# Optimization experiments

Hardware: AMD Instinct MI355X
Metric: run time of the kernel (lower is better)

Reference implementation:

```python
import jax, jax.numpy as jnp
import numpy as np

B, N, NINP, NFEAT, H = 4096, 4096, 64, 32, 4


def setup_inputs() -> dict:
    key = jax.random.key(0)
    ks = jax.random.split(key, 8)
    s_in = 1.0 / np.sqrt(NINP)
    s_att = 1.0 / np.sqrt(2 * NFEAT)
    return {
        "X": jax.random.normal(ks[0], (B, NINP), jnp.float32),
        "G": jax.random.normal(ks[1], (N, NINP), jnp.float32),
        "A": jax.random.uniform(ks[2], (B, N), jnp.float32),  # additive mask
        "W": jax.random.uniform(ks[3], (H, NINP, NFEAT), jnp.float32, -s_in, s_in),
        "b": jax.random.uniform(ks[4], (H, NFEAT), jnp.float32, -s_in, s_in),
        "a_src": jax.random.uniform(ks[5], (H, NFEAT), jnp.float32, -s_att, s_att),
        "a_dst": jax.random.uniform(ks[6], (H, NFEAT), jnp.float32, -s_att, s_att),
        "att_b": jax.random.uniform(ks[7], (H,), jnp.float32, -s_att, s_att),
    }


def reference(X, G, A, W, b, a_src, a_dst, att_b):
    # Per-head linear transforms (all heads batched via einsum)
    WX = jnp.einsum("bi,hif->bhf", X, W) + b            # (B, H, F)
    WG = jnp.einsum("ni,hif->nhf", G, W) + b            # (N, H, F)
    # Decomposed concat-attention: a^T [WX_b ; WG_n] = a_src.WX_b + a_dst.WG_n
    s_src = jnp.einsum("bhf,hf->bh", WX, a_src)         # (B, H)
    s_dst = jnp.einsum("nhf,hf->nh", WG, a_dst)         # (N, H)
    e = s_src[:, :, None] + s_dst.T[None, :, :] + att_b[None, :, None]  # (B,H,N)
    att = jax.nn.softmax(e - A[:, None, :], axis=-1)    # adjacency-masked softmax
    # Dropout(0.5) is identity in eval mode (deterministic reference).
    out = jnp.einsum("bhn,nhf->bhf", att, WG)           # weighted aggregation
    out = jax.nn.relu(out)                              # activation before concat
    return out.reshape(out.shape[0], -1)                # (B, H*F) concat heads
```

## Files before the change

### kernel.cpp

```cpp
#include <hip/hip_runtime.h>
#include <stdint.h>

#define N_TOK 4096
#define D_IN  64
#define NF    32
#define NH    4
#define OUTW  (NH * NF)
#define NT    8
#define CHUNK 128
#define BT    32

typedef float        f32x4  __attribute__((ext_vector_type(4)));
typedef unsigned int uint4v __attribute__((ext_vector_type(4)));
typedef __bf16       bf16x8 __attribute__((ext_vector_type(8)));

union Frag { uint4v u; bf16x8 v; };

static __device__ __forceinline__ unsigned short f2bf_rne(float x) {
  unsigned u = __float_as_uint(x);
  u += 0x7fffu + ((u >> 16) & 1u);
  return (unsigned short)(u >> 16);
}
static __device__ __forceinline__ float bflo(unsigned x) {
  return __uint_as_float(x << 16);
}
static __device__ __forceinline__ float bfhi(unsigned x) {
  return __uint_as_float(x & 0xffff0000u);
}

__global__ __launch_bounds__(128) void prep_kernel(
    const float* __restrict__ G, const float* __restrict__ W,
    const float* __restrict__ bias, const float* __restrict__ a_dst,
    unsigned short* __restrict__ EDH, unsigned short* __restrict__ PB) {
  __shared__ float gs[NT * D_IN];
  const int tid = threadIdx.x;
  const int n0  = blockIdx.x * NT;
  {
    const float4* src = (const float4*)(G + (size_t)n0 * D_IN);
    float4* dst = (float4*)gs;
    dst[tid] = src[tid];
  }
  __syncthreads();
  const int h = tid >> 5, f = tid & 31;
  float acc[NT];
  const float bb = bias[h * NF + f];
#pragma unroll
  for (int k = 0; k < NT; ++k) acc[k] = bb;
#pragma unroll
  for (int i = 0; i < D_IN; ++i) {
    const float wv = W[(h * D_IN + i) * NF + f];
#pragma unroll
    for (int k = 0; k < NT; ++k) acc[k] = fmaf(gs[k * D_IN + i], wv, acc[k]);
  }
  const float ad = a_dst[h * NF + f];
  float ev[NT];
#pragma unroll
  for (int k = 0; k < NT; ++k) {
    float s = acc[k] * ad;
    s += __shfl_xor(s, 1);  s += __shfl_xor(s, 2);  s += __shfl_xor(s, 4);
    s += __shfl_xor(s, 8);  s += __shfl_xor(s, 16);
    ev[k] = __expf(s);
  }
  const int t   = n0 >> 5;
  const int gq  = (n0 >> 3) & 3;
  const int set = (h << 1) | (f >> 4);
  const int col = f & 15;
  union { uint4 u4; unsigned short us[8]; } pk;
#pragma unroll
  for (int k = 0; k < NT; ++k) pk.us[k] = f2bf_rne(acc[k] * ev[k]);
  *(uint4*)(PB + (size_t)((((t * 8 + set) << 6) + (gq << 4) + col)) * 8) = pk.u4;
  if (f == 0) {
    union { uint4 u4; unsigned short us[8]; } pe;
#pragma unroll
    for (int k = 0; k < NT; ++k) pe.us[k] = f2bf_rne(ev[k]);
    *(uint4*)&EDH[(size_t)h * N_TOK + n0] = pe.u4;
  }
}

template <int NS>
__global__ __launch_bounds__(512) void attn_kernel(
    const float* __restrict__ A, const unsigned short* __restrict__ EDH,
    const unsigned short* __restrict__ PB, float* __restrict__ op,
    float* __restrict__ dp, float* __restrict__ out) {
  constexpr int NHALF  = N_TOK / NS;
  constexpr int NIT    = NHALF / CHUNK;
  constexpr int RINGSZ = BT * CHUNK * 2;
  __shared__ __align__(16) unsigned short ring[3 * BT * CHUNK];
  __shared__ __align__(16) unsigned short EDt[NH * NHALF];
  __shared__ float denLds[BT * NH];
  char* ringb = (char*)ring;

  const int tid  = threadIdx.x;
  const int lane = tid & 63;
  const int w    = tid >> 6;
  const int bid  = blockIdx.x;
  const int s    = bid & (NS - 1);
  const int b0   = (bid / NS) * BT;

  const int srow = tid >> 4, tp = tid & 15;
  const float* abase = A + (size_t)(b0 + srow) * N_TOK + s * NHALF + tp * 8;
  const int wb0 = srow * 256 + ((tp ^ (srow & 15)) << 4);

  const int rowm = lane & 15, g = lane >> 4;
  const char* pbb  = (const char*)PB + (size_t)s * (NHALF / 32) * 8192;
  const char* pown = pbb + (((w << 6) + lane) << 4);

  {
    const uint4* src = (const uint4*)EDH;
    uint4* dst = (uint4*)EDt;
    constexpr int tot = NH * NHALF / 8;
#pragma unroll 1
    for (int i = tid; i < tot; i += 512) {
      const int hh = i / (NHALF / 8), k = i % (NHALF / 8);
      dst[i] = src[hh * (N_TOK / 8) + s * (NHALF / 8) + k];
    }
  }
  __syncthreads();

  f32x4 acc0 = {0.f, 0.f, 0.f, 0.f}, acc1 = {0.f, 0.f, 0.f, 0.f};
  f32x4 dsum = {0.f, 0.f, 0.f, 0.f};
  f32x4 aXa, aXb, aYa, aYb;
  Frag bo0, bo1, bo2, bo3, co0, co1, co2, co3;
  int mR = 0, mW = 1;

#define LOADA2(d0, d1, cc) do {                                                \
    const float* ap_ = abase + (size_t)(cc) * CHUNK;                           \
    asm volatile("global_load_dwordx4 %0, %1, off"                            \
                 : "=v"(d0) : "v"(ap_) : "memory");                            \
    asm volatile("global_load_dwordx4 %0, %1, off"                            \
                 : "=v"(d1) : "v"(ap_ + 4) : "memory");                        \
  } while (0)
#define LOADB(fr, cc, kk)                                                      \
  asm volatile("global_load_dwordx4 %0, %1, off"                              \
               : "=v"(fr.u)                                                    \
               : "v"(pown + (size_t)((cc) * 4 + (kk)) * 8192) : "memory")

#define EXPP(AV0, AV1, cchunk, mw) do {                                        \
    float x0 = __expf(-AV0[0]), x1 = __expf(-AV0[1]);                          \
    float x2 = __expf(-AV0[2]), x3 = __expf(-AV0[3]);                          \
    float x4 = __expf(-AV1[0]), x5 = __expf(-AV1[1]);                          \
    float x6 = __expf(-AV1[2]), x7 = __expf(-AV1[3]);                          \
    if ((cchunk) < NIT) {                                                      \
      const int eo_ = (cchunk) * CHUNK + tp * 8;                               \
      uint4v e0_ = *(const uint4v*)&EDt[0 * NHALF + eo_];                      \
      uint4v e1_ = *(const uint4v*)&EDt[1 * NHALF + eo_];                      \
      uint4v e2_ = *(const uint4v*)&EDt[2 * NHALF + eo_];                      \
      uint4v e3_ = *(const uint4v*)&EDt[3 * NHALF + eo_];                      \
      dsum[0] = fmaf(x0, bflo(e0_[0]), dsum[0]);                               \
      dsum[0] = fmaf(x1, bfhi(e0_[0]), dsum[0]);                               \
      dsum[0] = fmaf(x2, bflo(e0_[1]), dsum[0]);                               \
      dsum[0] = fmaf(x3, bfhi(e0_[1]), dsum[0]);                               \
      dsum[0] = fmaf(x4, bflo(e0_[2]), dsum[0]);                               \
      dsum[0] = fmaf(x5, bfhi(e0_[2]), dsum[0]);                               \
      dsum[0] = fmaf(x6, bflo(e0_[3]), dsum[0]);                               \
      dsum[0] = fmaf(x7, bfhi(e0_[3]), dsum[0]);                               \
      dsum[1] = fmaf(x0, bflo(e1_[0]), dsum[1]);                               \
      dsum[1] = fmaf(x1, bfhi(e1_[0]), dsum[1]);                               \
      dsum[1] = fmaf(x2, bflo(e1_[1]), dsum[1]);                               \
      dsum[1] = fmaf(x3, bfhi(e1_[1]), dsum[1]);                               \
      dsum[1] = fmaf(x4, bflo(e1_[2]), dsum[1]);                               \
      dsum[1] = fmaf(x5, bfhi(e1_[2]), dsum[1]);                               \
      dsum[1] = fmaf(x6, bflo(e1_[3]), dsum[1]);                               \
      dsum[1] = fmaf(x7, bfhi(e1_[3]), dsum[1]);                               \
      dsum[2] = fmaf(x0, bflo(e2_[0]), dsum[2]);                               \
      dsum[2] = fmaf(x1, bfhi(e2_[0]), dsum[2]);                               \
      dsum[2] = fmaf(x2, bflo(e2_[1]), dsum[2]);                               \
      dsum[2] = fmaf(x3, bfhi(e2_[1]), dsum[2]);                               \
      dsum[2] = fmaf(x4, bflo(e2_[2]), dsum[2]);                               \
      dsum[2] = fmaf(x5, bfhi(e2_[2]), dsum[2]);                               \
      dsum[2] = fmaf(x6, bflo(e2_[3]), dsum[2]);                               \
      dsum[2] = fmaf(x7, bfhi(e2_[3]), dsum[2]);                               \
      dsum[3] = fmaf(x0, bflo(e3_[0]), dsum[3]);                               \
      dsum[3] = fmaf(x1, bfhi(e3_[0]), dsum[3]);                               \
      dsum[3] = fmaf(x2, bflo(e3_[1]), dsum[3]);                               \
      dsum[3] = fmaf(x3, bfhi(e3_[1]), dsum[3]);                               \
      dsum[3] = fmaf(x4, bflo(e3_[2]), dsum[3]);                               \
      dsum[3] = fmaf(x5, bfhi(e3_[2]), dsum[3]);                               \
      dsum[3] = fmaf(x6, bflo(e3_[3]), dsum[3]);                               \
      dsum[3] = fmaf(x7, bfhi(e3_[3]), dsum[3]);                               \
    }                                                                          \
    uint4v t_;                                                                 \
    t_[0] = __builtin_amdgcn_perm(__float_as_uint(x1), __float_as_uint(x0), 0x07060302u); \
    t_[1] = __builtin_amdgcn_perm(__float_as_uint(x3), __float_as_uint(x2), 0x07060302u); \
    t_[2] = __builtin_amdgcn_perm(__float_as_uint(x5), __float_as_uint(x4), 0x07060302u); \
    t_[3] = __builtin_amdgcn_perm(__float_as_uint(x7), __float_as_uint(x6), 0x07060302u); \
    *(uint4v*)(ringb + (mw) * RINGSZ + wb0) = t_;                              \
  } while (0)

#define MSTEP(rg, kk, FB) do {                                                 \
    Frag af_;                                                                  \
    af_.v = *(const bf16x8*)(ringb + mR * RINGSZ + ((rg) * 16 + rowm) * 256 +  \
                             ((((kk) * 4 + g) ^ rowm) << 4));                  \
    if ((rg) == 0)                                                             \
      acc0 = __builtin_amdgcn_mfma_f32_16x16x32_bf16(af_.v, FB.v, acc0, 0, 0, 0); \
    else                                                                       \
      acc1 = __builtin_amdgcn_mfma_f32_16x16x32_bf16(af_.v, FB.v, acc1, 0, 0, 0); \
  } while (0)

#define ITER(cc, AC0, AC1, AN0, AN1, CO0, CO1, CO2, CO3,                       \
             NO0, NO1, NO2, NO3) do {                                          \
    { const int cb_ = ((cc) + 1 < NIT) ? (cc) + 1 : NIT - 1;                   \
      LOADB(NO0, cb_, 0); LOADB(NO1, cb_, 1);                                  \
      LOADB(NO2, cb_, 2); LOADB(NO3, cb_, 3); }                                \
    { const int ca_ = ((cc) + 2 < NIT) ? (cc) + 2 : NIT - 1;                   \
      LOADA2(AN0, AN1, ca_); }                                                 \
    asm volatile("s_waitcnt vmcnt(6)" ::: "memory");                           \
    __builtin_amdgcn_sched_barrier(0);                                         \
    EXPP(AC0, AC1, (cc) + 1, mW);                                              \
    asm volatile("s_waitcnt lgkmcnt(0)" ::: "memory");                         \
    __builtin_amdgcn_sched_barrier(0);                                         \
    __builtin_amdgcn_s_barrier();                                              \
    MSTEP(0, 0, CO0); MSTEP(1, 0, CO0);                                        \
    MSTEP(0, 1, CO1); MSTEP(1, 1, CO1);                                        \
    MSTEP(0, 2, CO2); MSTEP(1, 2, CO2);                                        \
    MSTEP(0, 3, CO3); MSTEP(1, 3, CO3);                                        \
    mR = mW; mW = (mW + 1 == 3) ? 0 : mW + 1;                                  \
  } while (0)

  LOADA2(aXa, aXb, 0);
  LOADB(bo0, 0, 0); LOADB(bo1, 0, 1); LOADB(bo2, 0, 2); LOADB(bo3, 0, 3);
  LOADA2(aYa, aYb, 1);
  asm volatile("s_waitcnt vmcnt(6)" ::: "memory");
  __builtin_amdgcn_sched_barrier(0);
  EXPP(aXa, aXb, 0, 0);

#pragma unroll 1
  for (int i = 0; i < NIT; i += 2) {
    ITER(i,     aYa, aYb, aXa, aXb, bo0, bo1, bo2, bo3, co0, co1, co2, co3);
    ITER(i + 1, aXa, aXb, aYa, aYb, co0, co1, co2, co3, bo0, bo1, bo2, bo3);
  }

  asm volatile("s_waitcnt vmcnt(0)" ::: "memory");
  __builtin_amdgcn_sched_barrier(0);

#pragma unroll
  for (int m = 1; m <= 8; m <<= 1) {
    dsum[0] += __shfl_xor(dsum[0], m);
    dsum[1] += __shfl_xor(dsum[1], m);
    dsum[2] += __shfl_xor(dsum[2], m);
    dsum[3] += __shfl_xor(dsum[3], m);
  }

  if (NS == 1) {
    if (tp == 0) {
      float4 dv; dv.x = dsum[0]; dv.y = dsum[1]; dv.z = dsum[2]; dv.w = dsum[3];
      *(float4*)&denLds[srow * NH] = dv;
    }
    __syncthreads();
    const int hh = w >> 1;
#pragma unroll
    for (int r = 0; r < 4; ++r) {
      const int rr = g * 4 + r;
      float o;
      o = acc0[r] / denLds[rr * NH + hh];
      out[(size_t)(b0 + rr) * OUTW + w * 16 + rowm] = o > 0.f ? o : 0.f;
      o = acc1[r] / denLds[(16 + rr) * NH + hh];
      out[(size_t)(b0 + 16 + rr) * OUTW + w * 16 + rowm] = o > 0.f ? o : 0.f;
    }
  } else {
    if (tp == 0) {
      float4 dv; dv.x = dsum[0]; dv.y = dsum[1]; dv.z = dsum[2]; dv.w = dsum[3];
      *(float4*)&dp[((size_t)s * N_TOK + b0 + srow) * NH] = dv;
    }
    float* ob = op + (size_t)s * (N_TOK * OUTW) + (size_t)b0 * OUTW + w * 16 + rowm;
#pragma unroll
    for (int r = 0; r < 4; ++r) {
      const int rr = g * 4 + r;
      ob[(size_t)rr * OUTW]        = acc0[r];
      ob[(size_t)(16 + rr) * OUTW] = acc1[r];
    }
  }
#undef LOADA2
#undef LOADB
#undef EXPP
#undef MSTEP
#undef ITER
}

__global__ __launch_bounds__(256) void comb_kernel(
    const float* __restrict__ op, const float* __restrict__ dp,
    float* __restrict__ out, int NS) {
  const int idx4 = blockIdx.x * 256 + threadIdx.x;
  const int eb = idx4 >> 5;
  const int h  = ((idx4 << 2) & 127) >> 5;
  float4 o; o.x = 0.f; o.y = 0.f; o.z = 0.f; o.w = 0.f;
  float d = 0.f;
  for (int s2 = 0; s2 < NS; ++s2) {
    float4 vv = *(const float4*)(op + (size_t)s2 * (N_TOK * OUTW) + (size_t)idx4 * 4);
    o.x += vv.x; o.y += vv.y; o.z += vv.z; o.w += vv.w;
    d += dp[((size_t)s2 * N_TOK + eb) * NH + h];
  }
  const float r = 1.f / d;
  float4 res;
  res.x = fmaxf(o.x * r, 0.f);
  res.y = fmaxf(o.y * r, 0.f);
  res.z = fmaxf(o.z * r, 0.f);
  res.w = fmaxf(o.w * r, 0.f);
  *(float4*)(out + (size_t)idx4 * 4) = res;
}

extern "C" void kernel_launch(void* const* d_in, const int* in_sizes, int n_in,
                              void* d_out, int out_size, void* d_ws, size_t ws_size,
                              hipStream_t stream) {
  const float* G     = (const float*)d_in[1];
  const float* A     = (const float*)d_in[2];
  const float* W     = (const float*)d_in[3];
  const float* bias  = (const float*)d_in[4];
  const float* a_dst = (const float*)d_in[6];

  char* ws = (char*)d_ws;
  const size_t PBsz = (size_t)128 * 8 * 1024;
  const size_t EDsz = (size_t)N_TOK * NH * 2;
  const size_t base = PBsz + EDsz;
  const size_t per_split = (size_t)N_TOK * OUTW * 4 + (size_t)N_TOK * NH * 4;

  unsigned short* PB  = (unsigned short*)ws;
  unsigned short* EDH = (unsigned short*)(ws + PBsz);
  float* op = (float*)(ws + base);
  float* outp = (float*)d_out;

  prep_kernel<<<N_TOK / NT, 128, 0, stream>>>(G, W, bias, a_dst, EDH, PB);
  if (ws_size >= base + 8 * per_split) {
    float* dp = (float*)(ws + base + 8 * (size_t)N_TOK * OUTW * 4);
    attn_kernel<8><<<(N_TOK / BT) * 8, 512, 0, stream>>>(A, EDH, PB, op, dp, nullptr);
    comb_kernel<<<(N_TOK * OUTW / 4) / 256, 256, 0, stream>>>(op, dp, outp, 8);
  } else if (ws_size >= base + 4 * per_split) {
    float* dp = (float*)(ws + base + 4 * (size_t)N_TOK * OUTW * 4);
    attn_kernel<4><<<(N_TOK / BT) * 4, 512, 0, stream>>>(A, EDH, PB, op, dp, nullptr);
    comb_kernel<<<(N_TOK * OUTW / 4) / 256, 256, 0, stream>>>(op, dp, outp, 4);
  } else if (ws_size >= base + 2 * per_split) {
    float* dp = (float*)(ws + base + 2 * (size_t)N_TOK * OUTW * 4);
    attn_kernel<2><<<(N_TOK / BT) * 2, 512, 0, stream>>>(A, EDH, PB, op, dp, nullptr);
    comb_kernel<<<(N_TOK * OUTW / 4) / 256, 256, 0, stream>>>(op, dp, outp, 2);
  } else {
    attn_kernel<1><<<N_TOK / BT, 512, 0, stream>>>(A, EDH, PB, nullptr, nullptr, outp);
  }
}
```

Before: 34.14 us.

## Halve attention block to 256 threads, each wave computing two output column tiles

The attention kernel now runs 4 waves per block instead of 8. Each wave owns two 16-column output tiles and reuses every LDS A-fragment for two MFMAs, so LDS reads per MFMA are halved. Each thread also exponentiates 16 mask values instead of 8. The B-fragment prefetch changes from double-buffered next-chunk loading to loading the current chunk inside the iteration, guarded by a vmcnt wait before the MFMAs. In exchange the kernel uses more registers per thread, has fewer waves to hide latency, and may expose the B-load latency.

```diff
diff --git a/kernel.cpp b/kernel.cpp
--- a/kernel.cpp
+++ b/kernel.cpp
@@ -78,7 +78,7 @@
 }
 
 template <int NS>
-__global__ __launch_bounds__(512) void attn_kernel(
+__global__ __launch_bounds__(256) void attn_kernel(
     const float* __restrict__ A, const unsigned short* __restrict__ EDH,
     const unsigned short* __restrict__ PB, float* __restrict__ op,
     float* __restrict__ dp, float* __restrict__ out) {
@@ -97,55 +97,65 @@
   const int s    = bid & (NS - 1);
   const int b0   = (bid / NS) * BT;
 
-  const int srow = tid >> 4, tp = tid & 15;
-  const float* abase = A + (size_t)(b0 + srow) * N_TOK + s * NHALF + tp * 8;
-  const int wb0 = srow * 256 + ((tp ^ (srow & 15)) << 4);
+  const int srow = tid >> 3, tp = tid & 7;
+  const float* abase = A + (size_t)(b0 + srow) * N_TOK + s * NHALF + tp * 16;
+  const int wb0 = srow * 256 + (((2 * tp    ) ^ (srow & 15)) << 4);
+  const int wb1 = srow * 256 + (((2 * tp + 1) ^ (srow & 15)) << 4);
 
   const int rowm = lane & 15, g = lane >> 4;
-  const char* pbb  = (const char*)PB + (size_t)s * (NHALF / 32) * 8192;
-  const char* pown = pbb + (((w << 6) + lane) << 4);
+  const char* pbb = (const char*)PB + (size_t)s * (NHALF / 32) * 8192;
+  const char* pw0 = pbb + ((((2 * w    ) << 6) + lane) << 4);
+  const char* pw1 = pbb + ((((2 * w + 1) << 6) + lane) << 4);
 
   {
     const uint4* src = (const uint4*)EDH;
     uint4* dst = (uint4*)EDt;
     constexpr int tot = NH * NHALF / 8;
 #pragma unroll 1
-    for (int i = tid; i < tot; i += 512) {
+    for (int i = tid; i < tot; i += 256) {
       const int hh = i / (NHALF / 8), k = i % (NHALF / 8);
       dst[i] = src[hh * (N_TOK / 8) + s * (NHALF / 8) + k];
     }
   }
   __syncthreads();
 
-  f32x4 acc0 = {0.f, 0.f, 0.f, 0.f}, acc1 = {0.f, 0.f, 0.f, 0.f};
+  f32x4 ac00 = {0.f, 0.f, 0.f, 0.f}, ac01 = {0.f, 0.f, 0.f, 0.f};
+  f32x4 ac10 = {0.f, 0.f, 0.f, 0.f}, ac11 = {0.f, 0.f, 0.f, 0.f};
   f32x4 dsum = {0.f, 0.f, 0.f, 0.f};
-  f32x4 aXa, aXb, aYa, aYb;
-  Frag bo0, bo1, bo2, bo3, co0, co1, co2, co3;
+  f32x4 aXa, aXb, aXc, aXd, aYa, aYb, aYc, aYd;
+  Frag f00, f01, f02, f03, f10, f11, f12, f13;
   int mR = 0, mW = 1;
 
-#define LOADA2(d0, d1, cc) do {                                                \
+#define LOADA4(d0, d1, d2, d3, cc) do {                                        \
     const float* ap_ = abase + (size_t)(cc) * CHUNK;                           \
     asm volatile("global_load_dwordx4 %0, %1, off"                            \
                  : "=v"(d0) : "v"(ap_) : "memory");                            \
     asm volatile("global_load_dwordx4 %0, %1, off"                            \
                  : "=v"(d1) : "v"(ap_ + 4) : "memory");                        \
-  } while (0)
-#define LOADB(fr, cc, kk)                                                      \
+    asm volatile("global_load_dwordx4 %0, %1, off"                            \
+                 : "=v"(d2) : "v"(ap_ + 8) : "memory");                        \
+    asm volatile("global_load_dwordx4 %0, %1, off"                            \
+                 : "=v"(d3) : "v"(ap_ + 12) : "memory");                       \
+  } while (0)
+#define LOADB0(fr, cc, kk)                                                     \
   asm volatile("global_load_dwordx4 %0, %1, off"                              \
                : "=v"(fr.u)                                                    \
-               : "v"(pown + (size_t)((cc) * 4 + (kk)) * 8192) : "memory")
-
-#define EXPP(AV0, AV1, cchunk, mw) do {                                        \
-    float x0 = __expf(-AV0[0]), x1 = __expf(-AV0[1]);                          \
-    float x2 = __expf(-AV0[2]), x3 = __expf(-AV0[3]);                          \
-    float x4 = __expf(-AV1[0]), x5 = __expf(-AV1[1]);                          \
-    float x6 = __expf(-AV1[2]), x7 = __expf(-AV1[3]);                          \
+               : "v"(pw0 + (size_t)((cc) * 4 + (kk)) * 8192) : "memory")
+#define LOADB1(fr, cc, kk)                                                     \
+  asm volatile("global_load_dwordx4 %0, %1, off"                              \
+               : "=v"(fr.u)                                                    \
+               : "v"(pw1 + (size_t)((cc) * 4 + (kk)) * 8192) : "memory")
+
+#define EXPH(P0, P1, eoff, wboff, cchunk, mw) do {                             \
+    float x0 = __expf(-P0[0]), x1 = __expf(-P0[1]);                            \
+    float x2 = __expf(-P0[2]), x3 = __expf(-P0[3]);                            \
+    float x4 = __expf(-P1[0]), x5 = __expf(-P1[1]);                            \
+    float x6 = __expf(-P1[2]), x7 = __expf(-P1[3]);                            \
     if ((cchunk) < NIT) {                                                      \
-      const int eo_ = (cchunk) * CHUNK + tp * 8;                               \
-      uint4v e0_ = *(const uint4v*)&EDt[0 * NHALF + eo_];                      \
-      uint4v e1_ = *(const uint4v*)&EDt[1 * NHALF + eo_];                      \
-      uint4v e2_ = *(const uint4v*)&EDt[2 * NHALF + eo_];                      \
-      uint4v e3_ = *(const uint4v*)&EDt[3 * NHALF + eo_];                      \
+      uint4v e0_ = *(const uint4v*)&EDt[0 * NHALF + (eoff)];                   \
+      uint4v e1_ = *(const uint4v*)&EDt[1 * NHALF + (eoff)];                   \
+      uint4v e2_ = *(const uint4v*)&EDt[2 * NHALF + (eoff)];                   \
+      uint4v e3_ = *(const uint4v*)&EDt[3 * NHALF + (eoff)];                   \
       dsum[0] = fmaf(x0, bflo(e0_[0]), dsum[0]);                               \
       dsum[0] = fmaf(x1, bfhi(e0_[0]), dsum[0]);                               \
       dsum[0] = fmaf(x2, bflo(e0_[1]), dsum[0]);                               \
@@ -184,57 +194,62 @@
     t_[1] = __builtin_amdgcn_perm(__float_as_uint(x3), __float_as_uint(x2), 0x07060302u); \
     t_[2] = __builtin_amdgcn_perm(__float_as_uint(x5), __float_as_uint(x4), 0x07060302u); \
     t_[3] = __builtin_amdgcn_perm(__float_as_uint(x7), __float_as_uint(x6), 0x07060302u); \
-    *(uint4v*)(ringb + (mw) * RINGSZ + wb0) = t_;                              \
-  } while (0)
-
-#define MSTEP(rg, kk, FB) do {                                                 \
+    *(uint4v*)(ringb + (mw) * RINGSZ + (wboff)) = t_;                          \
+  } while (0)
+
+#define EXPP(P0, P1, P2, P3, cchunk, mw) do {                                  \
+    const int eo_ = (cchunk) < NIT ? (cchunk) * CHUNK + tp * 16 : 0;           \
+    EXPH(P0, P1, eo_, wb0, cchunk, mw);                                        \
+    EXPH(P2, P3, eo_ + 8, wb1, cchunk, mw);                                    \
+  } while (0)
+
+#define MSTEP2(AC0, AC1, rg, kk, FB0, FB1) do {                                \
     Frag af_;                                                                  \
     af_.v = *(const bf16x8*)(ringb + mR * RINGSZ + ((rg) * 16 + rowm) * 256 +  \
                              ((((kk) * 4 + g) ^ rowm) << 4));                  \
-    if ((rg) == 0)                                                             \
-      acc0 = __builtin_amdgcn_mfma_f32_16x16x32_bf16(af_.v, FB.v, acc0, 0, 0, 0); \
-    else                                                                       \
-      acc1 = __builtin_amdgcn_mfma_f32_16x16x32_bf16(af_.v, FB.v, acc1, 0, 0, 0); \
-  } while (0)
-
-#define ITER(cc, AC0, AC1, AN0, AN1, CO0, CO1, CO2, CO3,                       \
-             NO0, NO1, NO2, NO3) do {                                          \
-    { const int cb_ = ((cc) + 1 < NIT) ? (cc) + 1 : NIT - 1;                   \
-      LOADB(NO0, cb_, 0); LOADB(NO1, cb_, 1);                                  \
-      LOADB(NO2, cb_, 2); LOADB(NO3, cb_, 3); }                                \
+    AC0 = __builtin_amdgcn_mfma_f32_16x16x32_bf16(af_.v, FB0.v, AC0, 0, 0, 0); \
+    AC1 = __builtin_amdgcn_mfma_f32_16x16x32_bf16(af_.v, FB1.v, AC1, 0, 0, 0); \
+  } while (0)
+
+#define ITER(cc, AU0, AU1, AU2, AU3, AL0, AL1, AL2, AL3) do {                  \
+    LOADB0(f00, cc, 0); LOADB0(f01, cc, 1);                                    \
+    LOADB0(f02, cc, 2); LOADB0(f03, cc, 3);                                    \
+    LOADB1(f10, cc, 0); LOADB1(f11, cc, 1);                                    \
+    LOADB1(f12, cc, 2); LOADB1(f13, cc, 3);                                    \
     { const int ca_ = ((cc) + 2 < NIT) ? (cc) + 2 : NIT - 1;                   \
-      LOADA2(AN0, AN1, ca_); }                                                 \
-    asm volatile("s_waitcnt vmcnt(6)" ::: "memory");                           \
+      LOADA4(AL0, AL1, AL2, AL3, ca_); }                                       \
+    asm volatile("s_waitcnt vmcnt(12)" ::: "memory");                          \
     __builtin_amdgcn_sched_barrier(0);                                         \
-    EXPP(AC0, AC1, (cc) + 1, mW);                                              \
+    EXPP(AU0, AU1, AU2, AU3, (cc) + 1, mW);                                    \
     asm volatile("s_waitcnt lgkmcnt(0)" ::: "memory");                         \
     __builtin_amdgcn_sched_barrier(0);                                         \
     __builtin_amdgcn_s_barrier();                                              \
-    MSTEP(0, 0, CO0); MSTEP(1, 0, CO0);                                        \
-    MSTEP(0, 1, CO1); MSTEP(1, 1, CO1);                                        \
-    MSTEP(0, 2, CO2); MSTEP(1, 2, CO2);                                        \
-    MSTEP(0, 3, CO3); MSTEP(1, 3, CO3);                                        \
+    asm volatile("s_waitcnt vmcnt(4)" ::: "memory");                           \
+    __builtin_amdgcn_sched_barrier(0);                                         \
+    MSTEP2(ac00, ac10, 0, 0, f00, f10); MSTEP2(ac01, ac11, 1, 0, f00, f10);    \
+    MSTEP2(ac00, ac10, 0, 1, f01, f11); MSTEP2(ac01, ac11, 1, 1, f01, f11);    \
+    MSTEP2(ac00, ac10, 0, 2, f02, f12); MSTEP2(ac01, ac11, 1, 2, f02, f12);    \
+    MSTEP2(ac00, ac10, 0, 3, f03, f13); MSTEP2(ac01, ac11, 1, 3, f03, f13);    \
     mR = mW; mW = (mW + 1 == 3) ? 0 : mW + 1;                                  \
   } while (0)
 
-  LOADA2(aXa, aXb, 0);
-  LOADB(bo0, 0, 0); LOADB(bo1, 0, 1); LOADB(bo2, 0, 2); LOADB(bo3, 0, 3);
-  LOADA2(aYa, aYb, 1);
-  asm volatile("s_waitcnt vmcnt(6)" ::: "memory");
+  LOADA4(aXa, aXb, aXc, aXd, 0);
+  LOADA4(aYa, aYb, aYc, aYd, (1 < NIT) ? 1 : 0);
+  asm volatile("s_waitcnt vmcnt(4)" ::: "memory");
   __builtin_amdgcn_sched_barrier(0);
-  EXPP(aXa, aXb, 0, 0);
+  EXPP(aXa, aXb, aXc, aXd, 0, 0);
 
 #pragma unroll 1
   for (int i = 0; i < NIT; i += 2) {
-    ITER(i,     aYa, aYb, aXa, aXb, bo0, bo1, bo2, bo3, co0, co1, co2, co3);
-    ITER(i + 1, aXa, aXb, aYa, aYb, co0, co1, co2, co3, bo0, bo1, bo2, bo3);
+    ITER(i,     aYa, aYb, aYc, aYd, aXa, aXb, aXc, aXd);
+    ITER(i + 1, aXa, aXb, aXc, aXd, aYa, aYb, aYc, aYd);
   }
 
   asm volatile("s_waitcnt vmcnt(0)" ::: "memory");
   __builtin_amdgcn_sched_barrier(0);
 
 #pragma unroll
-  for (int m = 1; m <= 8; m <<= 1) {
+  for (int m = 1; m <= 4; m <<= 1) {
     dsum[0] += __shfl_xor(dsum[0], m);
     dsum[1] += __shfl_xor(dsum[1], m);
     dsum[2] += __shfl_xor(dsum[2], m);
@@ -247,33 +262,42 @@
       *(float4*)&denLds[srow * NH] = dv;
     }
     __syncthreads();
-    const int hh = w >> 1;
 #pragma unroll
     for (int r = 0; r < 4; ++r) {
       const int rr = g * 4 + r;
+      const float d0 = denLds[rr * NH + w];
+      const float d1 = denLds[(16 + rr) * NH + w];
       float o;
-      o = acc0[r] / denLds[rr * NH + hh];
-      out[(size_t)(b0 + rr) * OUTW + w * 16 + rowm] = o > 0.f ? o : 0.f;
-      o = acc1[r] / denLds[(16 + rr) * NH + hh];
-      out[(size_t)(b0 + 16 + rr) * OUTW + w * 16 + rowm] = o > 0.f ? o : 0.f;
+      o = ac00[r] / d0;
+      out[(size_t)(b0 + rr) * OUTW + w * 32 + rowm] = o > 0.f ? o : 0.f;
+      o = ac01[r] / d1;
+      out[(size_t)(b0 + 16 + rr) * OUTW + w * 32 + rowm] = o > 0.f ? o : 0.f;
+      o = ac10[r] / d0;
+      out[(size_t)(b0 + rr) * OUTW + w * 32 + 16 + rowm] = o > 0.f ? o : 0.f;
+      o = ac11[r] / d1;
+      out[(size_t)(b0 + 16 + rr) * OUTW + w * 32 + 16 + rowm] = o > 0.f ? o : 0.f;
     }
   } else {
     if (tp == 0) {
       float4 dv; dv.x = dsum[0]; dv.y = dsum[1]; dv.z = dsum[2]; dv.w = dsum[3];
       *(float4*)&dp[((size_t)s * N_TOK + b0 + srow) * NH] = dv;
     }
-    float* ob = op + (size_t)s * (N_TOK * OUTW) + (size_t)b0 * OUTW + w * 16 + rowm;
+    float* ob = op + (size_t)s * (N_TOK * OUTW) + (size_t)b0 * OUTW + w * 32 + rowm;
 #pragma unroll
     for (int r = 0; r < 4; ++r) {
       const int rr = g * 4 + r;
-      ob[(size_t)rr * OUTW]        = acc0[r];
-      ob[(size_t)(16 + rr) * OUTW] = acc1[r];
-    }
-  }
-#undef LOADA2
-#undef LOADB
+      ob[(size_t)rr * OUTW]             = ac00[r];
+      ob[(size_t)(16 + rr) * OUTW]      = ac01[r];
+      ob[(size_t)rr * OUTW + 16]        = ac10[r];
+      ob[(size_t)(16 + rr) * OUTW + 16] = ac11[r];
+    }
+  }
+#undef LOADA4
+#undef LOADB0
+#undef LOADB1
+#undef EXPH
 #undef EXPP
-#undef MSTEP
+#undef MSTEP2
 #undef ITER
 }
 
@@ -322,17 +346,17 @@
   prep_kernel<<<N_TOK / NT, 128, 0, stream>>>(G, W, bias, a_dst, EDH, PB);
   if (ws_size >= base + 8 * per_split) {
     float* dp = (float*)(ws + base + 8 * (size_t)N_TOK * OUTW * 4);
-    attn_kernel<8><<<(N_TOK / BT) * 8, 512, 0, stream>>>(A, EDH, PB, op, dp, nullptr);
+    attn_kernel<8><<<(N_TOK / BT) * 8, 256, 0, stream>>>(A, EDH, PB, op, dp, nullptr);
     comb_kernel<<<(N_TOK * OUTW / 4) / 256, 256, 0, stream>>>(op, dp, outp, 8);
   } else if (ws_size >= base + 4 * per_split) {
     float* dp = (float*)(ws + base + 4 * (size_t)N_TOK * OUTW * 4);
-    attn_kernel<4><<<(N_TOK / BT) * 4, 512, 0, stream>>>(A, EDH, PB, op, dp, nullptr);
+    attn_kernel<4><<<(N_TOK / BT) * 4, 256, 0, stream>>>(A, EDH, PB, op, dp, nullptr);
     comb_kernel<<<(N_TOK * OUTW / 4) / 256, 256, 0, stream>>>(op, dp, outp, 4);
   } else if (ws_size >= base + 2 * per_split) {
     float* dp = (float*)(ws + base + 2 * (size_t)N_TOK * OUTW * 4);
-    attn_kernel<2><<<(N_TOK / BT) * 2, 512, 0, stream>>>(A, EDH, PB, op, dp, nullptr);
+    attn_kernel<2><<<(N_TOK / BT) * 2, 256, 0, stream>>>(A, EDH, PB, op, dp, nullptr);
     comb_kernel<<<(N_TOK * OUTW / 4) / 256, 256, 0, stream>>>(op, dp, outp, 2);
   } else {
-    attn_kernel<1><<<N_TOK / BT, 512, 0, stream>>>(A, EDH, PB, nullptr, nullptr, outp);
-  }
-}
+    attn_kernel<1><<<N_TOK / BT, 256, 0, stream>>>(A, EDH, PB, nullptr, nullptr, outp);
+  }
+}
```

Measured after the change: 35.30 us. 1.03x slower.
